# Kernel optimization log

Measured on AMD Instinct MI355X. Metric: run time of the kernel, lower is better.

## Reference

```python
import jax, jax.numpy as jnp
import numpy as np

H = 4  # num_heads in all three MultiheadAttention layers


def _mha(x, valid, Wq, Wk, Wv, Wo, bq, bk, bv, bo):
    """Batched self-attention with key_padding_mask, matching torch MHA math.
    x: [..., L, D]; valid: [..., L] float (1=real token, 0=pad)."""
    lead = x.shape[:-2]
    L, D = x.shape[-2], x.shape[-1]
    dh = D // H
    q = (x @ Wq + bq).reshape(*lead, L, H, dh)
    k = (x @ Wk + bk).reshape(*lead, L, H, dh)
    v = (x @ Wv + bv).reshape(*lead, L, H, dh)
    scores = jnp.einsum('...qhd,...khd->...hqk', q, k) / jnp.sqrt(jnp.asarray(dh, x.dtype))
    neg = jnp.asarray(-1e9, x.dtype)  # finite so fully-masked rows stay NaN-free
    scores = jnp.where(valid[..., None, None, :] > 0, scores, neg)
    a = jax.nn.softmax(scores, axis=-1)
    o = jnp.einsum('...hqk,...khd->...qhd', a, v).reshape(*lead, L, D)
    return o @ Wo + bo


def _masked_mean(x, m):
    # (x * m).sum over sequence / (m.sum + 1e-10); fully-masked -> exact zeros,
    # matching the torch zeros() fallback branch.
    mm = m[..., None]
    return (x * mm).sum(-2) / (mm.sum(-2) + 1e-10)


def setup_inputs() -> dict:
    key = jax.random.key(0)
    B, S, N, W, D = 16, 8, 16, 64, 256
    ks = jax.random.split(key, 16)
    inp = {
        'word_embeddings': jax.random.normal(ks[0], (B, S, N, W, D), dtype=jnp.float32),
        'attention_mask': jax.random.randint(ks[1], (B, S, N, W), 0, 2).astype(jnp.int32),
    }
    i = 2
    for lvl in 'wsc':  # word / sentence / section attention params
        for p in ('Wq', 'Wk', 'Wv', 'Wo'):
            inp[lvl + p] = 0.02 * jax.random.normal(ks[i], (D, D), dtype=jnp.float32)
            i += 1
        for p in ('bq', 'bk', 'bv', 'bo'):
            inp[lvl + p] = jnp.zeros((D,), jnp.float32)
    return inp


def reference(word_embeddings, attention_mask,
              wWq, wWk, wWv, wWo, wbq, wbk, wbv, wbo,
              sWq, sWk, sWv, sWo, sbq, sbk, sbv, sbo,
              cWq, cWk, cWv, cWo, cbq, cbk, cbv, cbo):
    dt = word_embeddings.dtype
    mask = attention_mask.astype(dt)                       # [B,S,N,W]
    # word level: attention within each sentence, then masked mean pooling
    wo = _mha(word_embeddings, mask, wWq, wWk, wWv, wWo, wbq, wbk, wbv, wbo)
    sent = _masked_mean(wo, mask)                          # [B,S,N,D]
    # sentence level
    sent_mask = (mask.sum(-1) > 0).astype(dt)              # [B,S,N]
    so = _mha(sent, sent_mask, sWq, sWk, sWv, sWo, sbq, sbk, sbv, sbo)
    sec = _masked_mean(so, sent_mask)                      # [B,S,D]
    # section level
    sec_mask = (mask.sum((-1, -2)) > 0).astype(dt)         # [B,S]
    co = _mha(sec, sec_mask, cWq, cWk, cWv, cWo, cbq, cbk, cbv, cbo)
    doc = _masked_mean(co, sec_mask)                       # [B,D]
    return doc
```

## Files before the change

### kernel.cpp

```cpp
#include <hip/hip_runtime.h>

constexpr int D = 256;

typedef __attribute__((ext_vector_type(8))) __bf16 bf16x8;
typedef __attribute__((ext_vector_type(4))) float f32x4;
typedef __attribute__((ext_vector_type(16))) float f32x16;

__device__ inline unsigned short f2b(float f) {
    unsigned u = __builtin_bit_cast(unsigned, f);
    u = (u + 0x7fffu + ((u >> 16) & 1u)) >> 16;
    return (unsigned short)u;
}
__device__ inline unsigned cvt_pk_bf16(float lo, float hi) {
    unsigned r;
    asm volatile("v_cvt_pk_bf16_f32 %0, %1, %2" : "=v"(r) : "v"(lo), "v"(hi));
    return r;
}
__device__ inline bf16x8 ld_frag(const void* p) {
    uint4 r = *(const uint4*)p;
    return __builtin_bit_cast(bf16x8, r);
}
template<int CTRL>
__device__ inline float dpp_f(float v) {
    return __builtin_bit_cast(float,
        __builtin_amdgcn_update_dpp(0, __builtin_bit_cast(int, v), CTRL, 0xf, 0xf, true));
}
__device__ inline float rsum16(float v) {
    v += dpp_f<0x121>(v);
    v += dpp_f<0x122>(v);
    v += dpp_f<0x124>(v);
    v += dpp_f<0x128>(v);
    return v;
}
__device__ inline float rmax16(float v) {
    v = fmaxf(v, dpp_f<0x121>(v));
    v = fmaxf(v, dpp_f<0x122>(v));
    v = fmaxf(v, dpp_f<0x124>(v));
    v = fmaxf(v, dpp_f<0x128>(v));
    return v;
}
constexpr float CE = 0.125f * 1.44269504f;

__global__ void prep_wt3(const float* __restrict__ q0, const float* __restrict__ k0,
                         const float* __restrict__ q1, const float* __restrict__ k1,
                         const float* __restrict__ q2, const float* __restrict__ k2,
                         unsigned short* __restrict__ WT) {
    const int b = blockIdx.x, k = threadIdx.x;
    const int lvl = b >> 9, c = b & 511;
    const float* Wq = (lvl == 0) ? q0 : (lvl == 1) ? q1 : q2;
    const float* Wk = (lvl == 0) ? k0 : (lvl == 1) ? k1 : k2;
    const float* W = (c < 256) ? Wq : Wk;
    WT[(size_t)b * 256 + k] = f2b(W[k * 256 + (c & 255)]);
}

__global__ __launch_bounds__(512, 4)
void word_attn(const float* __restrict__ X, const int* __restrict__ Mask,
               const unsigned short* __restrict__ WT,
               const float* __restrict__ bq, const float* __restrict__ bk,
               float* __restrict__ Zout, float* __restrict__ Cnt)
{
    __shared__ unsigned short sKX[64 * 256];
    __shared__ unsigned short sQ[64 * 256];
    __shared__ float sM[64];
    __shared__ float sPart[8][64];
    __shared__ float sAbarT[64][4];
    __shared__ float sCt;

    const int tid = threadIdx.x;
    const int blk = blockIdx.x;
    const float* Xs = X + (size_t)blk * 64 * D;
    char* sKXb = (char*)sKX;
    char* sQb  = (char*)sQ;
    const int lane = tid & 63, w = tid >> 6;
    const int l31 = lane & 31, hi = lane >> 5;

    {
        const float4* X4 = (const float4*)Xs;
        float4 xv[8];
        #pragma unroll
        for (int j = 0; j < 8; ++j) xv[j] = X4[tid + j * 512];
        if (tid < 64) sM[tid] = (float)Mask[(size_t)blk * 64 + tid];
        #pragma unroll
        for (int j = 0; j < 8; ++j) {
            uint2 p;
            p.x = cvt_pk_bf16(xv[j].x, xv[j].y);
            p.y = cvt_pk_bf16(xv[j].z, xv[j].w);
            const int row = w + 8 * j;
            *(uint2*)(sKXb + row * 512 + ((lane * 8) ^ ((row & 7) << 4))) = p;
        }
    }
    const unsigned short* wtp = WT + (size_t)(w * 64 + l31) * 256 + hi * 8;
    bf16x8 aA[2], aB[2], aC[2], aD[2], b0[2], b1[2];
#define LDA(buf, kkv) { buf[0] = ld_frag(wtp + (kkv) * 16); buf[1] = ld_frag(wtp + 8192 + (kkv) * 16); }
#define LDB(buf, kkv) { \
        buf[0] = ld_frag(sKXb + l31 * 512 + (((kkv) * 32 + hi * 16) ^ ((l31 & 7) << 4))); \
        buf[1] = ld_frag(sKXb + (32 + l31) * 512 + (((kkv) * 32 + hi * 16) ^ (((32 + l31) & 7) << 4))); }
    LDA(aA, 0); LDA(aB, 1); LDA(aC, 2);
    __syncthreads();
    if (tid < 64) {
        float v = sM[tid];
        #pragma unroll
        for (int o = 1; o < 64; o <<= 1) v += __shfl_xor(v, o);
        if (tid == 0) sCt = v;
    }

    f32x16 acc[2][2];
    {
        const float* bias = (w < 4) ? bq : bk;
        const int fb = (w & 3) * 64;
        #pragma unroll
        for (int mf = 0; mf < 2; ++mf)
            #pragma unroll
            for (int g = 0; g < 4; ++g) {
                float4 b4 = *(const float4*)(bias + fb + mf * 32 + 8 * g + 4 * hi);
                #pragma unroll
                for (int nt = 0; nt < 2; ++nt) {
                    acc[mf][nt][4 * g + 0] = b4.x;
                    acc[mf][nt][4 * g + 1] = b4.y;
                    acc[mf][nt][4 * g + 2] = b4.z;
                    acc[mf][nt][4 * g + 3] = b4.w;
                }
            }
#define MFMA4(a, b) { \
        acc[0][0] = __builtin_amdgcn_mfma_f32_32x32x16_bf16(a[0], b[0], acc[0][0], 0, 0, 0); \
        acc[0][1] = __builtin_amdgcn_mfma_f32_32x32x16_bf16(a[0], b[1], acc[0][1], 0, 0, 0); \
        acc[1][0] = __builtin_amdgcn_mfma_f32_32x32x16_bf16(a[1], b[0], acc[1][0], 0, 0, 0); \
        acc[1][1] = __builtin_amdgcn_mfma_f32_32x32x16_bf16(a[1], b[1], acc[1][1], 0, 0, 0); }
#define PSTEP(ab, bb, an, ka, bn, kb, da, db) { \
        if (da) LDA(an, ka); \
        if (db) LDB(bn, kb); \
        __builtin_amdgcn_s_setprio(1); \
        MFMA4(ab, bb); \
        __builtin_amdgcn_s_setprio(0); }
        LDB(b0, 0);
        PSTEP(aA, b0, aD,  3, b1,  1, 1, 1);
        PSTEP(aB, b1, aA,  4, b0,  2, 1, 1);
        PSTEP(aC, b0, aB,  5, b1,  3, 1, 1);
        PSTEP(aD, b1, aC,  6, b0,  4, 1, 1);
        PSTEP(aA, b0, aD,  7, b1,  5, 1, 1);
        PSTEP(aB, b1, aA,  8, b0,  6, 1, 1);
        PSTEP(aC, b0, aB,  9, b1,  7, 1, 1);
        PSTEP(aD, b1, aC, 10, b0,  8, 1, 1);
        PSTEP(aA, b0, aD, 11, b1,  9, 1, 1);
        PSTEP(aB, b1, aA, 12, b0, 10, 1, 1);
        PSTEP(aC, b0, aB, 13, b1, 11, 1, 1);
        PSTEP(aD, b1, aC, 14, b0, 12, 1, 1);
        PSTEP(aA, b0, aD, 15, b1, 13, 1, 1);
        PSTEP(aB, b1, aA,  0, b0, 14, 0, 1);
        PSTEP(aC, b0, aB,  0, b1, 15, 0, 1);
        PSTEP(aD, b1, aC,  0, b0,  0, 0, 0);
    }
    auto WRITEBACK = [&](char* region) {
        #pragma unroll
        for (int nt = 0; nt < 2; ++nt) {
            const int t = nt * 32 + l31;
            char* rowp = region + t * 512;
            const int sw = (t & 7) << 4;
            #pragma unroll
            for (int mf = 0; mf < 2; ++mf)
                #pragma unroll
                for (int g = 0; g < 4; ++g) {
                    uint2 v;
                    v.x = cvt_pk_bf16(acc[mf][nt][4 * g + 0], acc[mf][nt][4 * g + 1]);
                    v.y = cvt_pk_bf16(acc[mf][nt][4 * g + 2], acc[mf][nt][4 * g + 3]);
                    const int fbyte = ((w & 3) * 64 + mf * 32 + 8 * g + 4 * hi) * 2;
                    *(uint2*)(rowp + (fbyte ^ sw)) = v;
                }
        }
    };
    if (w < 4) WRITEBACK(sQb);
    __syncthreads();
    if (w >= 4) WRITEBACK(sKXb);
    __syncthreads();

    {
        const int h = w >> 1, qh = w & 1;
        const int q = qh * 32 + l31;
        f32x16 sc0 = {}, sc1 = {};
        const int qsw = (q & 7) << 4;
        #pragma unroll
        for (int kk = 0; kk < 4; ++kk) {
            const int fby = h * 128 + kk * 32 + hi * 16;
            bf16x8 qa  = ld_frag(sQb + q * 512 + (fby ^ qsw));
            bf16x8 kb0 = ld_frag(sKXb + l31 * 512 + (fby ^ ((l31 & 7) << 4)));
            bf16x8 kb1 = ld_frag(sKXb + (32 + l31) * 512 + (fby ^ ((l31 & 7) << 4)));
            __builtin_amdgcn_s_setprio(1);
            sc0 = __builtin_amdgcn_mfma_f32_32x32x16_bf16(qa, kb0, sc0, 0, 0, 0);
            sc1 = __builtin_amdgcn_mfma_f32_32x32x16_bf16(qa, kb1, sc1, 0, 0, 0);
            __builtin_amdgcn_s_setprio(0);
        }
        const bool k0ok = sM[l31] > 0.f, k1ok = sM[32 + l31] > 0.f;
        float pm0 = 0.f, pm1 = 0.f;
        #pragma unroll
        for (int r = 0; r < 16; ++r) {
            const int qrow = qh * 32 + (r & 3) + 8 * (r >> 2) + 4 * hi;
            float e0 = k0ok ? __builtin_amdgcn_exp2f(sc0[r] * CE) : 0.f;
            float e1 = k1ok ? __builtin_amdgcn_exp2f(sc1[r] * CE) : 0.f;
            float se = rsum16(e0 + e1);
            se += __shfl_xor(se, 16);
            const float wr = sM[qrow] * __builtin_amdgcn_rcpf(se);
            pm0 += e0 * wr; pm1 += e1 * wr;
        }
        pm0 += __shfl_xor(pm0, 32);
        pm1 += __shfl_xor(pm1, 32);
        if (lane < 32) { sPart[w][lane] = pm0; sPart[w][32 + lane] = pm1; }
    }
    __syncthreads();
    if (tid < 256) {
        int h = tid >> 6, j = tid & 63;
        sAbarT[j][h] = sPart[2 * h][j] + sPart[2 * h + 1][j];
    }
    __syncthreads();

    float zp[4][4];
    #pragma unroll
    for (int h = 0; h < 4; ++h)
        #pragma unroll
        for (int e = 0; e < 4; ++e) zp[h][e] = 0.f;
    {
        const float4* X4 = (const float4*)Xs;
        float4 xz[8];
        #pragma unroll
        for (int j = 0; j < 8; ++j) xz[j] = X4[(w + 8 * j) * 64 + lane];
        #pragma unroll
        for (int j = 0; j < 8; ++j) {
            const int t = w + 8 * j;
            f32x4 ab = *(const f32x4*)&sAbarT[t][0];
            #pragma unroll
            for (int h = 0; h < 4; ++h) {
                zp[h][0] = fmaf(ab[h], xz[j].x, zp[h][0]);
                zp[h][1] = fmaf(ab[h], xz[j].y, zp[h][1]);
                zp[h][2] = fmaf(ab[h], xz[j].z, zp[h][2]);
                zp[h][3] = fmaf(ab[h], xz[j].w, zp[h][3]);
            }
        }
    }
    float* zr = (float*)sKXb;
    #pragma unroll
    for (int h = 0; h < 4; ++h)
        *(f32x4*)&zr[(w * 4 + h) * 256 + lane * 4] =
            (f32x4){zp[h][0], zp[h][1], zp[h][2], zp[h][3]};
    __syncthreads();
    {
        const int d = tid & 255, hp = (tid >> 8) * 2;
        float a0 = 0.f, a1 = 0.f;
        #pragma unroll
        for (int ww = 0; ww < 8; ++ww) {
            a0 += zr[(ww * 4 + hp) * 256 + d];
            a1 += zr[(ww * 4 + hp + 1) * 256 + d];
        }
        float* Zo = Zout + (size_t)blk * 1024;
        Zo[hp * 256 + d] = a0;
        Zo[(hp + 1) * 256 + d] = a1;
    }
    if (tid == 0) Cnt[blk] = sCt;
#undef LDA
#undef LDB
#undef MFMA4
#undef PSTEP
}

__global__ __launch_bounds__(512, 2)
void apply2(const float* __restrict__ Z, const float* __restrict__ Cnt,
            const float* __restrict__ Wv, const float* __restrict__ Wo,
            const float* __restrict__ bv, const float* __restrict__ bo,
            float* __restrict__ Out, float* __restrict__ MaskOut)
{
    constexpr int SPB = 8;
    __shared__ float sZ[SPB][4][256];
    __shared__ float sPP[SPB][256];
    __shared__ float sH[2][SPB][256];
    __shared__ float sCt[SPB];

    const int tid = threadIdx.x;
    const int s0 = blockIdx.x * SPB;
    {
        const float4* Zf = (const float4*)(Z + (size_t)s0 * 1024);
        float4* sZf = (float4*)sZ;
        #pragma unroll
        for (int k = 0; k < 4; ++k) sZf[tid + k * 512] = Zf[tid + k * 512];
        if (tid < SPB) sCt[tid] = Cnt[s0 + tid];
    }
    __syncthreads();

    const int n = tid & 255, g = tid >> 8, h = n >> 6;

    {
        float pa[SPB] = {};
        for (int dc = 0; dc < 128; dc += 16) {
            float wv[16];
            #pragma unroll
            for (int q = 0; q < 16; ++q) wv[q] = Wv[(size_t)(g * 128 + dc + q) * 256 + n];
            #pragma unroll
            for (int s = 0; s < SPB; ++s) {
                const float4* zp4 = (const float4*)&sZ[s][h][g * 128 + dc];
                #pragma unroll
                for (int q4 = 0; q4 < 4; ++q4) {
                    float4 zv = zp4[q4];
                    pa[s] = fmaf(zv.x, wv[q4 * 4 + 0], pa[s]);
                    pa[s] = fmaf(zv.y, wv[q4 * 4 + 1], pa[s]);
                    pa[s] = fmaf(zv.z, wv[q4 * 4 + 2], pa[s]);
                    pa[s] = fmaf(zv.w, wv[q4 * 4 + 3], pa[s]);
                }
            }
        }
        #pragma unroll
        for (int s = 0; s < SPB; ++s) sH[g][s][n] = pa[s];
    }
    __syncthreads();
    for (int i = tid; i < SPB * 256; i += 512) {
        int s = i >> 8, nn = i & 255;
        sPP[s][nn] = sH[0][s][nn] + sH[1][s][nn] + sCt[s] * bv[nn];
    }
    __syncthreads();
    {
        float pa[SPB] = {};
        for (int dc = 0; dc < 128; dc += 16) {
            float wo[16];
            #pragma unroll
            for (int q = 0; q < 16; ++q) wo[q] = Wo[(size_t)(g * 128 + dc + q) * 256 + n];
            #pragma unroll
            for (int s = 0; s < SPB; ++s) {
                const float4* pp = (const float4*)&sPP[s][g * 128 + dc];
                #pragma unroll
                for (int q4 = 0; q4 < 4; ++q4) {
                    float4 pv = pp[q4];
                    pa[s] = fmaf(pv.x, wo[q4 * 4 + 0], pa[s]);
                    pa[s] = fmaf(pv.y, wo[q4 * 4 + 1], pa[s]);
                    pa[s] = fmaf(pv.z, wo[q4 * 4 + 2], pa[s]);
                    pa[s] = fmaf(pv.w, wo[q4 * 4 + 3], pa[s]);
                }
            }
        }
        #pragma unroll
        for (int s = 0; s < SPB; ++s) sH[g][s][n] = pa[s];
    }
    __syncthreads();
    for (int i = tid; i < SPB * 256; i += 512) {
        int s = i >> 8, nn = i & 255;
        float c = sCt[s];
        Out[(size_t)(s0 + s) * 256 + nn] = (c > 0.f) ? ((sH[0][s][nn] + sH[1][s][nn]) / c + bo[nn]) : 0.f;
    }
    if (tid < SPB && MaskOut) MaskOut[s0 + tid] = (sCt[tid] > 0.f) ? 1.f : 0.f;
}

template<int LREAL>
__global__ __launch_bounds__(512, 2)
void tail_kernel(const float* __restrict__ X, const float* __restrict__ MaskIn,
                 const unsigned short* __restrict__ WT,
                 const float* __restrict__ bq, const float* __restrict__ bk,
                 const float* __restrict__ Wv, const float* __restrict__ Wo,
                 const float* __restrict__ bv, const float* __restrict__ bo,
                 float* __restrict__ Out, float* __restrict__ MaskOut)
{
    __shared__ unsigned short sX[16 * 256];
    __shared__ unsigned short sQK[16 * 512];
    __shared__ float sXF[16][256];
    __shared__ float sM[16];
    __shared__ float sAbar[4][16];
    __shared__ float sZp[2][4][256];
    __shared__ float sPP[256];
    __shared__ float sHH[2][256];
    __shared__ float sCt;

    const int tid = threadIdx.x;
    const int seq = blockIdx.x;
    const float* Xs = X + (size_t)seq * LREAL * 256;
    char* sBX = (char*)sX;
    char* sBQ = (char*)sQK;
    const int lane = tid & 63, w = tid >> 6;
    const int lr = lane & 15, lg = lane >> 4;

    {
        const float4* X4 = (const float4*)Xs;
        #pragma unroll
        for (int j = 0; j < 2; ++j) {
            int idx = tid + j * 512;
            int row = idx >> 6, c4 = idx & 63;
            float4 v = (row < LREAL) ? X4[row * 64 + c4] : (float4){0.f, 0.f, 0.f, 0.f};
            uint2 p;
            p.x = cvt_pk_bf16(v.x, v.y);
            p.y = cvt_pk_bf16(v.z, v.w);
            *(uint2*)(sBX + row * 512 + ((c4 * 8) ^ ((row & 7) << 4))) = p;
            *(float4*)&sXF[row][c4 * 4] = v;
        }
        if (tid < 16) sM[tid] = (tid < LREAL) ? MaskIn[seq * LREAL + tid] : 0.f;
    }
    const unsigned short* wtp = WT + (size_t)(w * 64 + lr) * 256 + lg * 8;
    bf16x8 afn[4];
    #pragma unroll
    for (int m = 0; m < 4; ++m) afn[m] = ld_frag(wtp + m * 16 * 256);
    __syncthreads();
    if (tid < 64) {
        float v = (lane < LREAL) ? sM[lane] : 0.f;
        v = rsum16(v);
        if (lane == 0) sCt = v;
    }

    f32x4 acc[4];
    {
        const float* bias = (w < 4) ? bq : bk;
        const int fb = (w & 3) * 64;
        #pragma unroll
        for (int m = 0; m < 4; ++m) {
            float4 b4 = *(const float4*)(bias + fb + m * 16 + lg * 4);
            acc[m] = (f32x4){b4.x, b4.y, b4.z, b4.w};
        }
        #pragma unroll 1
        for (int kk = 0; kk < 8; ++kk) {
            bf16x8 af[4];
            #pragma unroll
            for (int m = 0; m < 4; ++m) af[m] = afn[m];
            if (kk < 7) {
                #pragma unroll
                for (int m = 0; m < 4; ++m) afn[m] = ld_frag(wtp + m * 16 * 256 + (kk + 1) * 32);
            }
            bf16x8 bx = ld_frag(sBX + lr * 512 + ((kk * 64 + lg * 16) ^ ((lr & 7) << 4)));
            #pragma unroll
            for (int m = 0; m < 4; ++m)
                acc[m] = __builtin_amdgcn_mfma_f32_16x16x32_bf16(af[m], bx, acc[m], 0, 0, 0);
        }
    }
    #pragma unroll
    for (int m = 0; m < 4; ++m) {
        uint2 qk;
        qk.x = cvt_pk_bf16(acc[m][0], acc[m][1]);
        qk.y = cvt_pk_bf16(acc[m][2], acc[m][3]);
        *(uint2*)(sBQ + lr * 1024 + ((w * 128 + m * 32 + lg * 8) ^ ((lr & 7) << 4))) = qk;
    }
    __syncthreads();

    if (w < 4) {
        const int h = w;
        f32x4 sacc = (f32x4){0.f, 0.f, 0.f, 0.f};
        #pragma unroll
        for (int kk = 0; kk < 2; ++kk) {
            bf16x8 qf = ld_frag(sBQ + lr * 1024 + ((h * 128 + kk * 64 + lg * 16) ^ ((lr & 7) << 4)));
            bf16x8 kf = ld_frag(sBQ + lr * 1024 + ((512 + h * 128 + kk * 64 + lg * 16) ^ ((lr & 7) << 4)));
            sacc = __builtin_amdgcn_mfma_f32_16x16x32_bf16(qf, kf, sacc, 0, 0, 0);
        }
        const float mkey = sM[lr];
        float t = 0.f;
        #pragma unroll
        for (int r = 0; r < 4; ++r) {
            const int qi = lg * 4 + r;
            float s = (mkey > 0.f) ? sacc[r] : -1e9f;
            float mx = rmax16(s);
            float e = __builtin_amdgcn_exp2f((s - mx) * CE);
            float se = rsum16(e);
            t += e * (sM[qi] * __builtin_amdgcn_rcpf(se));
        }
        t += __shfl_xor(t, 16);
        t += __shfl_xor(t, 32);
        if (lane < 16) sAbar[h][lane] = t;
    }
    __syncthreads();

    {
        const int d = tid & 255, rh = tid >> 8;
        float zz[4] = {0.f, 0.f, 0.f, 0.f};
        #pragma unroll
        for (int t = 0; t < 8; ++t) {
            const int tok = rh * 8 + t;
            float xv = sXF[tok][d];
            #pragma unroll
            for (int h = 0; h < 4; ++h) zz[h] = fmaf(sAbar[h][tok], xv, zz[h]);
        }
        #pragma unroll
        for (int h = 0; h < 4; ++h) sZp[rh][h][d] = zz[h];
    }
    __syncthreads();

    const int n = tid & 255, g = tid >> 8, h = n >> 6;
    {
        float pa = 0.f;
        for (int dc = 0; dc < 128; dc += 16) {
            float wv[16];
            #pragma unroll
            for (int q = 0; q < 16; ++q) wv[q] = Wv[(size_t)(g * 128 + dc + q) * 256 + n];
            #pragma unroll
            for (int q = 0; q < 16; ++q) {
                int dd = g * 128 + dc + q;
                pa = fmaf(sZp[0][h][dd] + sZp[1][h][dd], wv[q], pa);
            }
        }
        sHH[g][n] = pa;
    }
    __syncthreads();
    if (tid < 256) sPP[tid] = sHH[0][tid] + sHH[1][tid] + sCt * bv[tid];
    __syncthreads();
    {
        float pa = 0.f;
        for (int dc = 0; dc < 128; dc += 16) {
            float wo[16];
            #pragma unroll
            for (int q = 0; q < 16; ++q) wo[q] = Wo[(size_t)(g * 128 + dc + q) * 256 + n];
            const float* pp = &sPP[g * 128 + dc];
            #pragma unroll
            for (int q = 0; q < 16; ++q) pa = fmaf(pp[q], wo[q], pa);
        }
        sHH[g][n] = pa;
    }
    __syncthreads();
    if (tid < 256) {
        float c = sCt;
        Out[(size_t)seq * 256 + tid] = (c > 0.f) ? ((sHH[0][tid] + sHH[1][tid]) / c + bo[tid]) : 0.f;
        if (MaskOut && tid == 0) MaskOut[seq] = (c > 0.f) ? 1.f : 0.f;
    }
}

extern "C" void kernel_launch(void* const* d_in, const int* in_sizes, int n_in,
                              void* d_out, int out_size, void* d_ws, size_t ws_size,
                              hipStream_t stream)
{
    const float* emb  = (const float*)d_in[0];
    const int*  amask = (const int*)d_in[1];
    const float* W[24];
    for (int i = 0; i < 24; ++i) W[i] = (const float*)d_in[2 + i];

    char* ws = (char*)d_ws;
    unsigned short* WT = (unsigned short*)ws;
    float* zbuf  = (float*)(ws + 3 * 256 * 1024);
    float* cnt   = zbuf + 2048 * 1024;
    float* sent  = cnt + 2048;
    float* smask = sent + 2048 * 256;
    float* sec   = smask + 2048;
    float* cmask = sec + 128 * 256;
    float* out   = (float*)d_out;

    prep_wt3<<<dim3(1536), dim3(256), 0, stream>>>(W[0], W[1], W[8], W[9], W[16], W[17], WT);

    word_attn<<<dim3(2048), dim3(512), 0, stream>>>(emb, amask, WT, W[4], W[5], zbuf, cnt);
    apply2<<<dim3(256), dim3(512), 0, stream>>>(zbuf, cnt, W[2], W[3], W[6], W[7], sent, smask);

    tail_kernel<16><<<dim3(128), dim3(512), 0, stream>>>(
        sent, smask, WT + 512 * 256, W[12], W[13], W[10], W[11], W[14], W[15], sec, cmask);

    tail_kernel<8><<<dim3(16), dim3(512), 0, stream>>>(
        sec, cmask, WT + 2 * 512 * 256, W[20], W[21], W[18], W[19], W[22], W[23], out, nullptr);
}
```

Measured before the change: 153.9 us.

## Keep Q in registers as MFMA fragments, reuse bf16 X from LDS for pooling

```diff
diff --git a/kernel.cpp b/kernel.cpp
--- a/kernel.cpp
+++ b/kernel.cpp
@@ -18,6 +18,10 @@
 }
 __device__ inline bf16x8 ld_frag(const void* p) {
     uint4 r = *(const uint4*)p;
+    return __builtin_bit_cast(bf16x8, r);
+}
+__device__ inline bf16x8 mk_frag(unsigned d0, unsigned d1, unsigned d2, unsigned d3) {
+    uint4 r = {d0, d1, d2, d3};
     return __builtin_bit_cast(bf16x8, r);
 }
 template<int CTRL>
@@ -59,18 +63,17 @@
                const float* __restrict__ bq, const float* __restrict__ bk,
                float* __restrict__ Zout, float* __restrict__ Cnt)
 {
-    __shared__ unsigned short sKX[64 * 256];
-    __shared__ unsigned short sQ[64 * 256];
+    __shared__ unsigned short sX[64 * 256];
+    __shared__ unsigned short sK[64 * 256];
     __shared__ float sM[64];
-    __shared__ float sPart[8][64];
     __shared__ float sAbarT[64][4];
     __shared__ float sCt;
 
     const int tid = threadIdx.x;
     const int blk = blockIdx.x;
     const float* Xs = X + (size_t)blk * 64 * D;
-    char* sKXb = (char*)sKX;
-    char* sQb  = (char*)sQ;
+    char* sXb = (char*)sX;
+    char* sKb = (char*)sK;
     const int lane = tid & 63, w = tid >> 6;
     const int l31 = lane & 31, hi = lane >> 5;
 
@@ -86,15 +89,15 @@
             p.x = cvt_pk_bf16(xv[j].x, xv[j].y);
             p.y = cvt_pk_bf16(xv[j].z, xv[j].w);
             const int row = w + 8 * j;
-            *(uint2*)(sKXb + row * 512 + ((lane * 8) ^ ((row & 7) << 4))) = p;
+            *(uint2*)(sXb + row * 512 + ((lane * 8) ^ ((row & 7) << 4))) = p;
         }
     }
     const unsigned short* wtp = WT + (size_t)(w * 64 + l31) * 256 + hi * 8;
     bf16x8 aA[2], aB[2], aC[2], aD[2], b0[2], b1[2];
 #define LDA(buf, kkv) { buf[0] = ld_frag(wtp + (kkv) * 16); buf[1] = ld_frag(wtp + 8192 + (kkv) * 16); }
 #define LDB(buf, kkv) { \
-        buf[0] = ld_frag(sKXb + l31 * 512 + (((kkv) * 32 + hi * 16) ^ ((l31 & 7) << 4))); \
-        buf[1] = ld_frag(sKXb + (32 + l31) * 512 + (((kkv) * 32 + hi * 16) ^ (((32 + l31) & 7) << 4))); }
+        buf[0] = ld_frag(sXb + l31 * 512 + (((kkv) * 32 + hi * 16) ^ ((l31 & 7) << 4))); \
+        buf[1] = ld_frag(sXb + (32 + l31) * 512 + (((kkv) * 32 + hi * 16) ^ ((l31 & 7) << 4))); }
     LDA(aA, 0); LDA(aB, 1); LDA(aC, 2);
     __syncthreads();
     if (tid < 64) {
@@ -150,11 +153,25 @@
         PSTEP(aC, b0, aB,  0, b1, 15, 0, 1);
         PSTEP(aD, b1, aC,  0, b0,  0, 0, 0);
     }
-    auto WRITEBACK = [&](char* region) {
+
+    bf16x8 qfrag[4][2];
+    if (w < 4) {
+        #pragma unroll
+        for (int kk = 0; kk < 4; ++kk) {
+            const int mf = kk >> 1, r0 = 8 * (kk & 1);
+            #pragma unroll
+            for (int i = 0; i < 2; ++i)
+                qfrag[kk][i] = mk_frag(
+                    cvt_pk_bf16(acc[mf][i][r0 + 0], acc[mf][i][r0 + 1]),
+                    cvt_pk_bf16(acc[mf][i][r0 + 2], acc[mf][i][r0 + 3]),
+                    cvt_pk_bf16(acc[mf][i][r0 + 4], acc[mf][i][r0 + 5]),
+                    cvt_pk_bf16(acc[mf][i][r0 + 6], acc[mf][i][r0 + 7]));
+        }
+    } else {
         #pragma unroll
         for (int nt = 0; nt < 2; ++nt) {
             const int t = nt * 32 + l31;
-            char* rowp = region + t * 512;
+            char* rowp = sKb + t * 512;
             const int sw = (t & 7) << 4;
             #pragma unroll
             for (int mf = 0; mf < 2; ++mf)
@@ -163,52 +180,55 @@
                     uint2 v;
                     v.x = cvt_pk_bf16(acc[mf][nt][4 * g + 0], acc[mf][nt][4 * g + 1]);
                     v.y = cvt_pk_bf16(acc[mf][nt][4 * g + 2], acc[mf][nt][4 * g + 3]);
-                    const int fbyte = ((w & 3) * 64 + mf * 32 + 8 * g + 4 * hi) * 2;
+                    const int fbyte = (w & 3) * 128 + 64 * mf + 32 * (g >> 1) + 16 * hi + 8 * (g & 1);
                     *(uint2*)(rowp + (fbyte ^ sw)) = v;
                 }
         }
-    };
-    if (w < 4) WRITEBACK(sQb);
-    __syncthreads();
-    if (w >= 4) WRITEBACK(sKXb);
-    __syncthreads();
-
-    {
-        const int h = w >> 1, qh = w & 1;
-        const int q = qh * 32 + l31;
-        f32x16 sc0 = {}, sc1 = {};
-        const int qsw = (q & 7) << 4;
+    }
+    __syncthreads();
+
+    if (w < 4) {
+        const int h = w;
+        f32x16 sc00 = {}, sc01 = {}, sc10 = {}, sc11 = {};
         #pragma unroll
         for (int kk = 0; kk < 4; ++kk) {
             const int fby = h * 128 + kk * 32 + hi * 16;
-            bf16x8 qa  = ld_frag(sQb + q * 512 + (fby ^ qsw));
-            bf16x8 kb0 = ld_frag(sKXb + l31 * 512 + (fby ^ ((l31 & 7) << 4)));
-            bf16x8 kb1 = ld_frag(sKXb + (32 + l31) * 512 + (fby ^ ((l31 & 7) << 4)));
+            bf16x8 kb0 = ld_frag(sKb + l31 * 512 + (fby ^ ((l31 & 7) << 4)));
+            bf16x8 kb1 = ld_frag(sKb + (32 + l31) * 512 + (fby ^ ((l31 & 7) << 4)));
             __builtin_amdgcn_s_setprio(1);
-            sc0 = __builtin_amdgcn_mfma_f32_32x32x16_bf16(qa, kb0, sc0, 0, 0, 0);
-            sc1 = __builtin_amdgcn_mfma_f32_32x32x16_bf16(qa, kb1, sc1, 0, 0, 0);
+            sc00 = __builtin_amdgcn_mfma_f32_32x32x16_bf16(qfrag[kk][0], kb0, sc00, 0, 0, 0);
+            sc01 = __builtin_amdgcn_mfma_f32_32x32x16_bf16(qfrag[kk][0], kb1, sc01, 0, 0, 0);
+            sc10 = __builtin_amdgcn_mfma_f32_32x32x16_bf16(qfrag[kk][1], kb0, sc10, 0, 0, 0);
+            sc11 = __builtin_amdgcn_mfma_f32_32x32x16_bf16(qfrag[kk][1], kb1, sc11, 0, 0, 0);
             __builtin_amdgcn_s_setprio(0);
         }
         const bool k0ok = sM[l31] > 0.f, k1ok = sM[32 + l31] > 0.f;
         float pm0 = 0.f, pm1 = 0.f;
-        #pragma unroll
-        for (int r = 0; r < 16; ++r) {
-            const int qrow = qh * 32 + (r & 3) + 8 * (r >> 2) + 4 * hi;
-            float e0 = k0ok ? __builtin_amdgcn_exp2f(sc0[r] * CE) : 0.f;
-            float e1 = k1ok ? __builtin_amdgcn_exp2f(sc1[r] * CE) : 0.f;
-            float se = rsum16(e0 + e1);
-            se += __shfl_xor(se, 16);
-            const float wr = sM[qrow] * __builtin_amdgcn_rcpf(se);
-            pm0 += e0 * wr; pm1 += e1 * wr;
-        }
+#define SMROW(SC0, SC1, itile) { \
+        _Pragma("unroll") \
+        for (int r = 0; r < 16; ++r) { \
+            const int qrow = 32 * (itile) + (r & 3) + 8 * (r >> 2) + 4 * hi; \
+            float e0 = k0ok ? __builtin_amdgcn_exp2f(SC0[r] * CE) : 0.f; \
+            float e1 = k1ok ? __builtin_amdgcn_exp2f(SC1[r] * CE) : 0.f; \
+            float se = rsum16(e0 + e1); \
+            se += __shfl_xor(se, 16); \
+            const float wr = sM[qrow] * __builtin_amdgcn_rcpf(se); \
+            pm0 += e0 * wr; pm1 += e1 * wr; } }
+        SMROW(sc00, sc01, 0)
+        SMROW(sc10, sc11, 1)
+#undef SMROW
         pm0 += __shfl_xor(pm0, 32);
         pm1 += __shfl_xor(pm1, 32);
-        if (lane < 32) { sPart[w][lane] = pm0; sPart[w][32 + lane] = pm1; }
-    }
-    __syncthreads();
-    if (tid < 256) {
-        int h = tid >> 6, j = tid & 63;
-        sAbarT[j][h] = sPart[2 * h][j] + sPart[2 * h + 1][j];
+        if (hi == 0) {
+            sAbarT[l31][h] = pm0;
+            sAbarT[32 + l31][h] = pm1;
+        }
+    }
+    uint2 xz[8];
+    #pragma unroll
+    for (int j = 0; j < 8; ++j) {
+        const int t = w + 8 * j;
+        xz[j] = *(const uint2*)(sXb + t * 512 + ((lane * 8) ^ ((t & 7) << 4)));
     }
     __syncthreads();
 
@@ -217,25 +237,23 @@
     for (int h = 0; h < 4; ++h)
         #pragma unroll
         for (int e = 0; e < 4; ++e) zp[h][e] = 0.f;
-    {
-        const float4* X4 = (const float4*)Xs;
-        float4 xz[8];
-        #pragma unroll
-        for (int j = 0; j < 8; ++j) xz[j] = X4[(w + 8 * j) * 64 + lane];
-        #pragma unroll
-        for (int j = 0; j < 8; ++j) {
-            const int t = w + 8 * j;
-            f32x4 ab = *(const f32x4*)&sAbarT[t][0];
-            #pragma unroll
-            for (int h = 0; h < 4; ++h) {
-                zp[h][0] = fmaf(ab[h], xz[j].x, zp[h][0]);
-                zp[h][1] = fmaf(ab[h], xz[j].y, zp[h][1]);
-                zp[h][2] = fmaf(ab[h], xz[j].z, zp[h][2]);
-                zp[h][3] = fmaf(ab[h], xz[j].w, zp[h][3]);
-            }
-        }
-    }
-    float* zr = (float*)sKXb;
+    #pragma unroll
+    for (int j = 0; j < 8; ++j) {
+        const int t = w + 8 * j;
+        f32x4 ab = *(const f32x4*)&sAbarT[t][0];
+        float x0 = __builtin_bit_cast(float, xz[j].x << 16);
+        float x1 = __builtin_bit_cast(float, xz[j].x & 0xffff0000u);
+        float x2 = __builtin_bit_cast(float, xz[j].y << 16);
+        float x3 = __builtin_bit_cast(float, xz[j].y & 0xffff0000u);
+        #pragma unroll
+        for (int h = 0; h < 4; ++h) {
+            zp[h][0] = fmaf(ab[h], x0, zp[h][0]);
+            zp[h][1] = fmaf(ab[h], x1, zp[h][1]);
+            zp[h][2] = fmaf(ab[h], x2, zp[h][2]);
+            zp[h][3] = fmaf(ab[h], x3, zp[h][3]);
+        }
+    }
+    float* zr = (float*)sKb;
     #pragma unroll
     for (int h = 0; h < 4; ++h)
         *(f32x4*)&zr[(w * 4 + h) * 256 + lane * 4] =
```

Result: faster. 148.2 us (-3.7%).
